# Kernel optimization log

Measured on AMD Instinct MI355X. Metric: run time of the kernel, lower is better.

## Reference

```python
import jax, jax.numpy as jnp
import numpy as np

RATIO = 1.0 / 32  # spacial_ratio
HOUT = 7          # pooled_h
WOUT = 7          # pooled_w
S = 2             # sub_bin_size = int(sqrt(n_sampled=4))


def setup_inputs() -> dict:
    key = jax.random.key(0)
    k1, k2, k3, k4, k5, k6 = jax.random.split(key, 6)
    B, C, H, W = 4, 256, 50, 50
    N = 1024
    img_w, img_h = W / RATIO, H / RATIO
    features = jax.random.normal(k1, (B, C, H, W), dtype=jnp.float32)
    b = jax.random.randint(k2, (N,), 0, B).astype(jnp.float32)
    x1 = jax.random.uniform(k3, (N,), minval=0.0, maxval=img_w - 232.0)
    y1 = jax.random.uniform(k4, (N,), minval=0.0, maxval=img_h - 232.0)
    bw = jax.random.uniform(k5, (N,), minval=32.0, maxval=232.0)
    bh = jax.random.uniform(k6, (N,), minval=32.0, maxval=232.0)
    rois = jnp.stack([b, x1, y1, x1 + bw, y1 + bh], axis=1)  # [N, 5]
    return {"features": features, "rois": rois}


def _roi_align(features, rois):
    B, C, H, W = features.shape
    fW = jnp.float32(W)
    fH = jnp.float32(H)
    b_idx = rois[:, 0].astype(jnp.int32)            # [N]
    box = rois[:, 1:] * RATIO                       # [N, 4] in feature coords
    bx1 = jnp.clip(box[:, 0], 0.0, fW)
    by1 = jnp.clip(box[:, 1], 0.0, fH)
    bx2 = jnp.clip(box[:, 2], 0.0, fW)
    by2 = jnp.clip(box[:, 3], 0.0, fH)
    roi_valid = (bx2 - bx1 > 0) & (by2 - by1 > 0)   # [N]
    bin_w = (bx2 - bx1) / WOUT                      # [N]
    bin_h = (by2 - by1) / HOUT

    jj = jnp.arange(WOUT, dtype=jnp.float32)
    ii = jnp.arange(HOUT, dtype=jnp.float32)
    # bin edges; y2/x2 computed from the UNclamped start, then clamped (matches original order)
    x1u = bx1[:, None] + jj * bin_w[:, None]        # [N, WOUT]
    x2b = jnp.clip(x1u + bin_w[:, None], 0.0, fW)
    x1b = jnp.clip(x1u, 0.0, fW)
    y1u = by1[:, None] + ii * bin_h[:, None]        # [N, HOUT]
    y2b = jnp.clip(y1u + bin_h[:, None], 0.0, fH)
    y1b = jnp.clip(y1u, 0.0, fH)
    bin_valid = (y2b > y1b)[:, :, None] & (x2b > x1b)[:, None, :]  # [N, HOUT, WOUT]

    # SxS sample-point centers inside each bin (sub_bin = bin / S, center offset 0.5)
    cc = jnp.arange(S, dtype=jnp.float32) + 0.5
    px = x1b[:, :, None] + cc * (bin_w / S)[:, None, None]  # [N, WOUT, S]
    py = y1b[:, :, None] + cc * (bin_h / S)[:, None, None]  # [N, HOUT, S]

    xl = jnp.clip(jnp.floor(px), 0, W - 1).astype(jnp.int32)
    xh = jnp.clip(xl + 1, 0, W - 1)
    yl = jnp.clip(jnp.floor(py), 0, H - 1).astype(jnp.int32)
    yh = jnp.clip(yl + 1, 0, H - 1)
    wxh = px - xl  # (x - x1)
    wxl = xh - px  # (x2 - x)
    wyb = py - yl  # (y - y1)
    wyt = yh - py  # (y2 - y)

    feats = features.transpose(0, 2, 3, 1)          # [B, H, W, C]
    bI = b_idx[:, None, None, None, None]           # [N,1,1,1,1]
    # x varies over (WOUT, sx) -> broadcast axes (2,4); y over (HOUT, sy) -> axes (1,3)
    XL = xl[:, None, :, None, :]
    XH = xh[:, None, :, None, :]
    YL = yl[:, :, None, :, None]
    YH = yh[:, :, None, :, None]
    WXh = wxh[:, None, :, None, :, None]
    WXl = wxl[:, None, :, None, :, None]
    WYb = wyb[:, :, None, :, None, None]
    WYt = wyt[:, :, None, :, None, None]

    v_tl = feats[bI, YL, XL]   # [N, HOUT, WOUT, S, S, C]
    v_tr = feats[bI, YL, XH]
    v_bl = feats[bI, YH, XL]
    v_br = feats[bI, YH, XH]
    top = WXh * v_tr + WXl * v_tl
    bot = WXh * v_br + WXl * v_bl
    val = WYb * bot + WYt * top                     # [N, HOUT, WOUT, S, S, C]

    pooled = val.max(axis=(3, 4))                   # max over sample grid -> [N, HOUT, WOUT, C]
    mask = bin_valid & roi_valid[:, None, None]
    pooled = jnp.where(mask[..., None], pooled, 0.0)
    return pooled.transpose(0, 3, 1, 2)             # [N, C, HOUT, WOUT]


def reference(features, rois):
    return _roi_align(features, rois)
```

## Files before the change

### kernel.cpp

```cpp
#include <hip/hip_runtime.h>


namespace {

constexpr int B_ = 4, C_ = 256, H_ = 50, W_ = 50;
constexpr int HW = H_ * W_;
constexpr int HO = 7, WO = 7, NBIN = HO * WO;
constexpr int OUT_PER_ROI = C_ * NBIN;
constexpr int LDH = 262;
constexpr float RATIO = 1.0f / 32.0f;

__device__ __forceinline__ unsigned short f2b(float x)
{
    unsigned u = __float_as_uint(x);
    u += 0x7fffu + ((u >> 16) & 1u);
    return (unsigned short)(u >> 16);
}

__device__ __forceinline__ float4 b2f(const uint2 r)
{
    float4 o;
    o.x = __uint_as_float(r.x << 16);
    o.y = __uint_as_float(r.x & 0xffff0000u);
    o.z = __uint_as_float(r.y << 16);
    o.w = __uint_as_float(r.y & 0xffff0000u);
    return o;
}

__global__ __launch_bounds__(256) void transpose_tiled(
    const float* __restrict__ f, unsigned short* __restrict__ ft)
{
    __shared__ float tile[64][65];
    const int bt   = blockIdx.x;
    const int hw_t = bt % 40;
    const int c_t  = (bt / 40) % 4;
    const int b    = bt / 160;
    const int hw0 = hw_t * 64, c0 = c_t * 64;
    const int lx = threadIdx.x & 63;
    const int ly = threadIdx.x >> 6;

#pragma unroll
    for (int k = 0; k < 16; ++k) {
        const int c  = c0 + k * 4 + ly;
        const int hw = hw0 + lx;
        if (hw < HW)
            tile[k * 4 + ly][lx] = f[((size_t)b * C_ + c) * HW + hw];
    }
    __syncthreads();

    const int pc = threadIdx.x & 31;
    const int pr = threadIdx.x >> 5;
#pragma unroll
    for (int k = 0; k < 8; ++k) {
        const int hwl = k * 8 + pr;
        const int hw  = hw0 + hwl;
        if (hw < HW) {
            const unsigned d = (unsigned)f2b(tile[2 * pc][hwl])
                             | ((unsigned)f2b(tile[2 * pc + 1][hwl]) << 16);
            *(unsigned*)&ft[((size_t)b * HW + hw) * C_ + c0 + 2 * pc] = d;
        }
    }
}

template<int AX, int AY>
__device__ __forceinline__ float4 do_bin(const uint2* __restrict__ pb2,
                                         const unsigned o[9],
                                         const float4 wa, const float4 wb)
{
    uint2 c[3][3];
#pragma unroll
    for (int j = 0; j < 2 + AY; ++j)
#pragma unroll
        for (int k = 0; k < 2 + AX; ++k)
            c[j][k] = pb2[o[j * 3 + k]];

    float4 h[3][2];
#pragma unroll
    for (int j = 0; j < 2 + AY; ++j) {
        const float4 p0 = b2f(c[j][0]);
        const float4 p1 = b2f(c[j][1]);
        const float4 lo1 = AX ? p1 : p0;
        const float4 hi1 = AX ? b2f(c[j][2]) : p1;
        h[j][0].x = wa.x * p1.x + wa.z * p0.x;
        h[j][0].y = wa.x * p1.y + wa.z * p0.y;
        h[j][0].z = wa.x * p1.z + wa.z * p0.z;
        h[j][0].w = wa.x * p1.w + wa.z * p0.w;
        h[j][1].x = wa.y * hi1.x + wa.w * lo1.x;
        h[j][1].y = wa.y * hi1.y + wa.w * lo1.y;
        h[j][1].z = wa.y * hi1.z + wa.w * lo1.z;
        h[j][1].w = wa.y * hi1.w + wa.w * lo1.w;
    }

    float4 m;
#pragma unroll
    for (int sy = 0; sy < 2; ++sy) {
        const float wyb = sy ? wb.y : wb.x;
        const float wyt = sy ? wb.w : wb.z;
        const int yj = AY * sy;
#pragma unroll
        for (int sx = 0; sx < 2; ++sx) {
            float4 s;
            s.x = wyb * h[yj + 1][sx].x + wyt * h[yj][sx].x;
            s.y = wyb * h[yj + 1][sx].y + wyt * h[yj][sx].y;
            s.z = wyb * h[yj + 1][sx].z + wyt * h[yj][sx].z;
            s.w = wyb * h[yj + 1][sx].w + wyt * h[yj][sx].w;
            if (sy == 0 && sx == 0) {
                m = s;
            } else {
                m.x = fmaxf(m.x, s.x);
                m.y = fmaxf(m.y, s.y);
                m.z = fmaxf(m.z, s.z);
                m.w = fmaxf(m.w, s.w);
            }
        }
    }
    return m;
}

__global__ __launch_bounds__(512, 8) void roialign_main(
    const unsigned short* __restrict__ ft,
    const float* __restrict__ rois,
    float* __restrict__ out)
{
    __shared__ unsigned short stageh[NBIN * LDH];
    __shared__ __align__(16) float    wts[NBIN][8];
    __shared__ __align__(16) unsigned offp[NBIN][12];

    const int n    = blockIdx.x;
    const int tid  = threadIdx.x;
    const int wave = tid >> 6;
    const int lane = tid & 63;
    const float fW = (float)W_, fH = (float)H_;

    if (tid < NBIN) {
        const int ii = tid / WO, jj = tid % WO;
        const float* r = rois + n * 5;
        const float bx1 = fminf(fmaxf(r[1] * RATIO, 0.0f), fW);
        const float by1 = fminf(fmaxf(r[2] * RATIO, 0.0f), fH);
        const float bx2 = fminf(fmaxf(r[3] * RATIO, 0.0f), fW);
        const float by2 = fminf(fmaxf(r[4] * RATIO, 0.0f), fH);
        const bool roi_valid = (bx2 - bx1 > 0.0f) && (by2 - by1 > 0.0f);
        const float bin_w = (bx2 - bx1) * (1.0f / (float)WO);
        const float bin_h = (by2 - by1) * (1.0f / (float)HO);

        const float x1u = bx1 + (float)jj * bin_w;
        const float x1b = fminf(fmaxf(x1u, 0.0f), fW);
        const float x2b = fminf(fmaxf(x1u + bin_w, 0.0f), fW);
        const float y1u = by1 + (float)ii * bin_h;
        const float y1b = fminf(fmaxf(y1u, 0.0f), fH);
        const float y2b = fminf(fmaxf(y1u + bin_h, 0.0f), fH);
        const float vf = (roi_valid && (y2b > y1b) && (x2b > x1b)) ? 1.0f : 0.0f;

        int xl[2], yl[2];
#pragma unroll
        for (int s = 0; s < 2; ++s) {
            const float px = x1b + ((float)s + 0.5f) * (bin_w * 0.5f);
            int l = (int)floorf(px);
            l = min(max(l, 0), W_ - 1);
            const int h = min(l + 1, W_ - 1);
            xl[s] = l;
            wts[tid][0 + s] = vf * (px - (float)l);
            wts[tid][2 + s] = vf * ((float)h - px);

            const float py = y1b + ((float)s + 0.5f) * (bin_h * 0.5f);
            int t = (int)floorf(py);
            t = min(max(t, 0), H_ - 1);
            const int u = min(t + 1, H_ - 1);
            yl[s] = t;
            wts[tid][4 + s] = py - (float)t;
            wts[tid][6 + s] = (float)u - py;
        }
        const int X0 = xl[0], Y0 = yl[0];
        const int ax = min(xl[1] - X0, 1);
        const int ay = min(yl[1] - Y0, 1);
        const int px_[3] = {X0, min(X0 + 1, W_ - 1), min(X0 + 2, W_ - 1)};
        const int py_[3] = {Y0, min(Y0 + 1, H_ - 1), min(Y0 + 2, H_ - 1)};
#pragma unroll
        for (int j = 0; j < 3; ++j)
#pragma unroll
            for (int k = 0; k < 3; ++k)
                offp[tid][j * 3 + k] = (unsigned)((py_[j] * W_ + px_[k]) << 6);
        offp[tid][9]  = (unsigned)(ax | (ay << 1));
        offp[tid][10] = 0u;
        offp[tid][11] = 0u;
    }

    int b = (int)rois[n * 5];
    b = min(max(b, 0), B_ - 1);
    const uint2* pb2 = (const uint2*)(ft + (size_t)b * HW * C_) + lane;

    __syncthreads();

    unsigned* const st32 = (unsigned*)stageh;
#pragma unroll
    for (int i = 0; i < 7; ++i) {
        const int bin = wave + 8 * i;
        if (bin < NBIN) {
            const float4 wa = *(const float4*)wts[bin];
            const float4 wb = *(const float4*)(wts[bin] + 4);
            const uint4 o0 = *(const uint4*)&offp[bin][0];
            const uint4 o1 = *(const uint4*)&offp[bin][4];
            const uint2 o2 = *(const uint2*)&offp[bin][8];
            const unsigned o[9] = {o0.x, o0.y, o0.z, o0.w,
                                   o1.x, o1.y, o1.z, o1.w, o2.x};
            const unsigned flags = __builtin_amdgcn_readfirstlane(o2.y);

            float4 m;
            switch (flags) {
                case 0u:  m = do_bin<0, 0>(pb2, o, wa, wb); break;
                case 1u:  m = do_bin<1, 0>(pb2, o, wa, wb); break;
                case 2u:  m = do_bin<0, 1>(pb2, o, wa, wb); break;
                default:  m = do_bin<1, 1>(pb2, o, wa, wb); break;
            }

            const unsigned lo = (unsigned)f2b(m.x) | ((unsigned)f2b(m.y) << 16);
            const unsigned hi = (unsigned)f2b(m.z) | ((unsigned)f2b(m.w) << 16);
            const int di = bin * (LDH / 2) + 2 * lane;
            st32[di]     = lo;
            st32[di + 1] = hi;
        }
    }
    __syncthreads();

    float* outn = out + (size_t)n * OUT_PER_ROI;
    for (int t = tid; t < OUT_PER_ROI / 2; t += 512) {
        const int k    = 2 * t;
        const int ch   = k / NBIN;
        const int bin  = k - ch * NBIN;
        const int ch2  = (bin + 1 < NBIN) ? ch : ch + 1;
        const int bin2 = (bin + 1 < NBIN) ? bin + 1 : 0;
        float2 v;
        v.x = __uint_as_float((unsigned)stageh[bin  * LDH + ch ] << 16);
        v.y = __uint_as_float((unsigned)stageh[bin2 * LDH + ch2] << 16);
        *(float2*)&outn[k] = v;
    }
}

}

extern "C" void kernel_launch(void* const* d_in, const int* in_sizes, int n_in,
                              void* d_out, int out_size, void* d_ws, size_t ws_size,
                              hipStream_t stream)
{
    const float* feats = (const float*)d_in[0];
    const float* rois  = (const float*)d_in[1];
    float* out = (float*)d_out;
    const int N = in_sizes[1] / 5;
    unsigned short* ft = (unsigned short*)d_ws;

    hipLaunchKernelGGL(transpose_tiled, dim3(B_ * 4 * 40), dim3(256), 0, stream,
                       feats, ft);
    hipLaunchKernelGGL(roialign_main, dim3(N), dim3(512), 0, stream,
                       ft, rois, out);
}
```

Before: 90.06 us.

## Fuse transpose into ROI kernel by staging a per-ROI feature patch in LDS

Removes the separate NCHW→NHWC bf16 transpose kernel. Each ROI block instead gathers a 10x10 spatial patch of all 256 channels straight from the fp32 NCHW features into shared memory as bf16. Bilinear sampling then reads neighbour offsets relative to that patch, and the block grows to 1024 threads. This saves a kernel launch and the global round-trip through the workspace. The cost is many redundant, less coalesced global reads of overlapping patches across ROIs, plus an extra barrier so the patch buffer can be reused for output staging.

```diff
diff --git a/kernel.cpp b/kernel.cpp
--- a/kernel.cpp
+++ b/kernel.cpp
@@ -7,6 +7,8 @@
 constexpr int HW = H_ * W_;
 constexpr int HO = 7, WO = 7, NBIN = HO * WO;
 constexpr int OUT_PER_ROI = C_ * NBIN;
+constexpr int PW = 10, PH = 10, NPOS = PW * PH;
+constexpr int PLD = 260;
 constexpr int LDH = 262;
 constexpr float RATIO = 1.0f / 32.0f;
 
@@ -27,43 +29,8 @@
     return o;
 }
 
-__global__ __launch_bounds__(256) void transpose_tiled(
-    const float* __restrict__ f, unsigned short* __restrict__ ft)
-{
-    __shared__ float tile[64][65];
-    const int bt   = blockIdx.x;
-    const int hw_t = bt % 40;
-    const int c_t  = (bt / 40) % 4;
-    const int b    = bt / 160;
-    const int hw0 = hw_t * 64, c0 = c_t * 64;
-    const int lx = threadIdx.x & 63;
-    const int ly = threadIdx.x >> 6;
-
-#pragma unroll
-    for (int k = 0; k < 16; ++k) {
-        const int c  = c0 + k * 4 + ly;
-        const int hw = hw0 + lx;
-        if (hw < HW)
-            tile[k * 4 + ly][lx] = f[((size_t)b * C_ + c) * HW + hw];
-    }
-    __syncthreads();
-
-    const int pc = threadIdx.x & 31;
-    const int pr = threadIdx.x >> 5;
-#pragma unroll
-    for (int k = 0; k < 8; ++k) {
-        const int hwl = k * 8 + pr;
-        const int hw  = hw0 + hwl;
-        if (hw < HW) {
-            const unsigned d = (unsigned)f2b(tile[2 * pc][hwl])
-                             | ((unsigned)f2b(tile[2 * pc + 1][hwl]) << 16);
-            *(unsigned*)&ft[((size_t)b * HW + hw) * C_ + c0 + 2 * pc] = d;
-        }
-    }
-}
-
 template<int AX, int AY>
-__device__ __forceinline__ float4 do_bin(const uint2* __restrict__ pb2,
+__device__ __forceinline__ float4 do_bin(const unsigned short* pbl,
                                          const unsigned o[9],
                                          const float4 wa, const float4 wb)
 {
@@ -72,7 +39,7 @@
     for (int j = 0; j < 2 + AY; ++j)
 #pragma unroll
         for (int k = 0; k < 2 + AX; ++k)
-            c[j][k] = pb2[o[j * 3 + k]];
+            c[j][k] = *(const uint2*)(pbl + o[j * 3 + k]);
 
     float4 h[3][2];
 #pragma unroll
@@ -117,12 +84,12 @@
     return m;
 }
 
-__global__ __launch_bounds__(512, 8) void roialign_main(
-    const unsigned short* __restrict__ ft,
+__global__ __launch_bounds__(1024, 8) void roialign_fused(
+    const float* __restrict__ f,
     const float* __restrict__ rois,
     float* __restrict__ out)
 {
-    __shared__ unsigned short stageh[NBIN * LDH];
+    __shared__ unsigned short patch[NPOS * PLD];
     __shared__ __align__(16) float    wts[NBIN][8];
     __shared__ __align__(16) unsigned offp[NBIN][12];
 
@@ -132,16 +99,38 @@
     const int lane = tid & 63;
     const float fW = (float)W_, fH = (float)H_;
 
+    const float* r = rois + n * 5;
+    const float bx1 = fminf(fmaxf(r[1] * RATIO, 0.0f), fW);
+    const float by1 = fminf(fmaxf(r[2] * RATIO, 0.0f), fH);
+    const float bx2 = fminf(fmaxf(r[3] * RATIO, 0.0f), fW);
+    const float by2 = fminf(fmaxf(r[4] * RATIO, 0.0f), fH);
+    const float bin_w = (bx2 - bx1) * (1.0f / (float)WO);
+    const float bin_h = (by2 - by1) * (1.0f / (float)HO);
+    const float px00 = bx1 + 0.5f * (bin_w * 0.5f);
+    const float py00 = by1 + 0.5f * (bin_h * 0.5f);
+    int X0 = (int)floorf(px00); X0 = min(max(X0, 0), W_ - 1);
+    int Y0 = (int)floorf(py00); Y0 = min(max(Y0, 0), H_ - 1);
+    int b = (int)r[0];
+    b = min(max(b, 0), B_ - 1);
+
+    {
+        const float* fb = f + (size_t)b * C_ * HW;
+        const int p0 = lane, p1 = 64 + lane;
+        const int yx0 = min(Y0 + p0 / PW, H_ - 1) * W_ + min(X0 + p0 % PW, W_ - 1);
+        const int yx1 = min(Y0 + p1 / PW, H_ - 1) * W_ + min(X0 + p1 % PW, W_ - 1);
+        const int cbase = wave << 4;
+#pragma unroll
+        for (int k = 0; k < 16; ++k) {
+            const float* fc = fb + (size_t)(cbase + k) * HW;
+            patch[p0 * PLD + cbase + k] = f2b(fc[yx0]);
+            if (lane < NPOS - 64)
+                patch[p1 * PLD + cbase + k] = f2b(fc[yx1]);
+        }
+    }
+
     if (tid < NBIN) {
         const int ii = tid / WO, jj = tid % WO;
-        const float* r = rois + n * 5;
-        const float bx1 = fminf(fmaxf(r[1] * RATIO, 0.0f), fW);
-        const float by1 = fminf(fmaxf(r[2] * RATIO, 0.0f), fH);
-        const float bx2 = fminf(fmaxf(r[3] * RATIO, 0.0f), fW);
-        const float by2 = fminf(fmaxf(r[4] * RATIO, 0.0f), fH);
         const bool roi_valid = (bx2 - bx1 > 0.0f) && (by2 - by1 > 0.0f);
-        const float bin_w = (bx2 - bx1) * (1.0f / (float)WO);
-        const float bin_h = (by2 - by1) * (1.0f / (float)HO);
 
         const float x1u = bx1 + (float)jj * bin_w;
         const float x1b = fminf(fmaxf(x1u, 0.0f), fW);
@@ -170,31 +159,30 @@
             wts[tid][4 + s] = py - (float)t;
             wts[tid][6 + s] = (float)u - py;
         }
-        const int X0 = xl[0], Y0 = yl[0];
-        const int ax = min(xl[1] - X0, 1);
-        const int ay = min(yl[1] - Y0, 1);
-        const int px_[3] = {X0, min(X0 + 1, W_ - 1), min(X0 + 2, W_ - 1)};
-        const int py_[3] = {Y0, min(Y0 + 1, H_ - 1), min(Y0 + 2, H_ - 1)};
+        const int Xb = xl[0], Yb = yl[0];
+        const int ax = min(xl[1] - Xb, 1);
+        const int ay = min(yl[1] - Yb, 1);
+        const int gx[3] = {Xb, min(Xb + 1, W_ - 1), min(Xb + 2, W_ - 1)};
+        const int gy[3] = {Yb, min(Yb + 1, H_ - 1), min(Yb + 2, H_ - 1)};
 #pragma unroll
         for (int j = 0; j < 3; ++j)
 #pragma unroll
-            for (int k = 0; k < 3; ++k)
-                offp[tid][j * 3 + k] = (unsigned)((py_[j] * W_ + px_[k]) << 6);
+            for (int k = 0; k < 3; ++k) {
+                const int ry = min(max(gy[j] - Y0, 0), PH - 1);
+                const int rx = min(max(gx[k] - X0, 0), PW - 1);
+                offp[tid][j * 3 + k] = (unsigned)((ry * PW + rx) * PLD);
+            }
         offp[tid][9]  = (unsigned)(ax | (ay << 1));
         offp[tid][10] = 0u;
         offp[tid][11] = 0u;
     }
-
-    int b = (int)rois[n * 5];
-    b = min(max(b, 0), B_ - 1);
-    const uint2* pb2 = (const uint2*)(ft + (size_t)b * HW * C_) + lane;
-
     __syncthreads();
 
-    unsigned* const st32 = (unsigned*)stageh;
-#pragma unroll
-    for (int i = 0; i < 7; ++i) {
-        const int bin = wave + 8 * i;
+    const unsigned short* pbl = patch + 4 * lane;
+    unsigned mlo[4], mhi[4];
+#pragma unroll
+    for (int i = 0; i < 4; ++i) {
+        const int bin = wave + 16 * i;
         if (bin < NBIN) {
             const float4 wa = *(const float4*)wts[bin];
             const float4 wb = *(const float4*)(wts[bin] + 4);
@@ -207,23 +195,32 @@
 
             float4 m;
             switch (flags) {
-                case 0u:  m = do_bin<0, 0>(pb2, o, wa, wb); break;
-                case 1u:  m = do_bin<1, 0>(pb2, o, wa, wb); break;
-                case 2u:  m = do_bin<0, 1>(pb2, o, wa, wb); break;
-                default:  m = do_bin<1, 1>(pb2, o, wa, wb); break;
+                case 0u:  m = do_bin<0, 0>(pbl, o, wa, wb); break;
+                case 1u:  m = do_bin<1, 0>(pbl, o, wa, wb); break;
+                case 2u:  m = do_bin<0, 1>(pbl, o, wa, wb); break;
+                default:  m = do_bin<1, 1>(pbl, o, wa, wb); break;
             }
-
-            const unsigned lo = (unsigned)f2b(m.x) | ((unsigned)f2b(m.y) << 16);
-            const unsigned hi = (unsigned)f2b(m.z) | ((unsigned)f2b(m.w) << 16);
+            mlo[i] = (unsigned)f2b(m.x) | ((unsigned)f2b(m.y) << 16);
+            mhi[i] = (unsigned)f2b(m.z) | ((unsigned)f2b(m.w) << 16);
+        }
+    }
+    __syncthreads();
+
+    unsigned* const st32 = (unsigned*)patch;
+#pragma unroll
+    for (int i = 0; i < 4; ++i) {
+        const int bin = wave + 16 * i;
+        if (bin < NBIN) {
             const int di = bin * (LDH / 2) + 2 * lane;
-            st32[di]     = lo;
-            st32[di + 1] = hi;
+            st32[di]     = mlo[i];
+            st32[di + 1] = mhi[i];
         }
     }
     __syncthreads();
 
+    unsigned short* const stageh = patch;
     float* outn = out + (size_t)n * OUT_PER_ROI;
-    for (int t = tid; t < OUT_PER_ROI / 2; t += 512) {
+    for (int t = tid; t < OUT_PER_ROI / 2; t += 1024) {
         const int k    = 2 * t;
         const int ch   = k / NBIN;
         const int bin  = k - ch * NBIN;
@@ -246,10 +243,8 @@
     const float* rois  = (const float*)d_in[1];
     float* out = (float*)d_out;
     const int N = in_sizes[1] / 5;
-    unsigned short* ft = (unsigned short*)d_ws;
-
-    hipLaunchKernelGGL(transpose_tiled, dim3(B_ * 4 * 40), dim3(256), 0, stream,
-                       feats, ft);
-    hipLaunchKernelGGL(roialign_main, dim3(N), dim3(512), 0, stream,
-                       ft, rois, out);
-}
+    (void)d_ws; (void)ws_size;
+
+    hipLaunchKernelGGL(roialign_fused, dim3(N), dim3(1024), 0, stream,
+                       feats, rois, out);
+}
```

Result: slower. 108.5 us (+20.4%).
